# Performance work log

Hardware: AMD Instinct MI355X
Metric: run time of the kernel (lower is better)

Reference implementation:

```python
import jax, jax.numpy as jnp
import numpy as np

H, W = 4096, 4096
KH, KW = 3, 3


def setup_inputs() -> dict:
    key = jax.random.key(0)
    k1, k2, k3 = jax.random.split(key, 3)
    X = jax.random.normal(k1, (H, W), dtype=jnp.float32)
    weight = jax.random.normal(k2, (KH, KW), dtype=jnp.float32)
    bias = jax.random.normal(k3, (1,), dtype=jnp.float32)
    return {"X": X, "weight": weight, "bias": bias}


def reference(X, weight, bias):
    # Valid 2D cross-correlation (no kernel flip), matching the torch double loop:
    # Y[i, j] = sum(X[i:i+h, j:j+w] * K) + bias
    lhs = X[None, None, :, :]          # NCHW
    rhs = weight[None, None, :, :]     # OIHW
    out = jax.lax.conv_general_dilated(
        lhs, rhs,
        window_strides=(1, 1),
        padding="VALID",
        dimension_numbers=("NCHW", "OIHW", "NCHW"),
    )
    return out[0, 0] + bias[0]  # [H-KH+1, W-KW+1]
```

## Files before the change

### kernel.cpp

```cpp
#include <hip/hip_runtime.h>


constexpr int Hin = 4096;
constexpr int Win = 4096;
constexpr int OH  = 4094;
constexpr int OW  = 4094;

constexpr int C = 8;
constexpr int R = 4;
constexpr int CT = 512;
constexpr int RT = 1024;

__global__ __launch_bounds__(256, 4) void conv3x3_kernel(
    const float* __restrict__ X, const float* __restrict__ Wt,
    const float* __restrict__ B, float* __restrict__ Out)
{
    int nb = gridDim.x;
    int b  = blockIdx.x;
    int b2 = (b & 7) * (nb >> 3) + (b >> 3);

    int t   = b2 * 256 + threadIdx.x;
    int cid = t & (CT - 1);
    int rid = t >> 9;
    int c0  = cid * C;
    int r0  = rid * R;

    int q2off = (c0 + 8 <= Win - 4) ? (c0 + 8) : (Win - 4);

    float4 q[6][3];
#pragma unroll
    for (int ir = 0; ir < 6; ++ir) {
        int rr = r0 + ir;
        if (rr > Hin - 1) rr = Hin - 1;
        const float* row = X + (size_t)rr * Win;
        q[ir][0] = *reinterpret_cast<const float4*>(row + c0);
        q[ir][1] = *reinterpret_cast<const float4*>(row + c0 + 4);
        q[ir][2] = *reinterpret_cast<const float4*>(row + q2off);
    }

    float w[9];
#pragma unroll
    for (int i = 0; i < 9; ++i) w[i] = Wt[i];
    const float bias = B[0];

    float acc[R][C];
#pragma unroll
    for (int i = 0; i < R; ++i)
#pragma unroll
        for (int j = 0; j < C; ++j) acc[i][j] = bias;

#pragma unroll
    for (int ir = 0; ir < 6; ++ir) {
        float v[12] = {q[ir][0].x, q[ir][0].y, q[ir][0].z, q[ir][0].w,
                       q[ir][1].x, q[ir][1].y, q[ir][1].z, q[ir][1].w,
                       q[ir][2].x, q[ir][2].y, q[ir][2].z, q[ir][2].w};
#pragma unroll
        for (int kh = 0; kh < 3; ++kh) {
            int orr = ir - kh;
            if (orr >= 0 && orr < R) {
#pragma unroll
                for (int kw = 0; kw < 3; ++kw) {
                    float wv = w[kh * 3 + kw];
#pragma unroll
                    for (int j = 0; j < C; ++j)
                        acc[orr][j] = fmaf(v[j + kw], wv, acc[orr][j]);
                }
            }
        }
    }

#pragma unroll
    for (int i = 0; i < R; ++i) {
        int orow = r0 + i;
        if (orow < OH) {
            size_t o = (size_t)orow * OW + c0;
#pragma unroll
            for (int p = 0; p < C / 2; ++p) {
                int col = c0 + 2 * p;
                if (col < OW) {
                    *reinterpret_cast<float2*>(Out + o + 2 * p) =
                        make_float2(acc[i][2 * p], acc[i][2 * p + 1]);
                }
            }
        }
    }
}

extern "C" void kernel_launch(void* const* d_in, const int* in_sizes, int n_in,
                              void* d_out, int out_size, void* d_ws, size_t ws_size,
                              hipStream_t stream) {
    const float* X  = (const float*)d_in[0];
    const float* Wt = (const float*)d_in[1];
    const float* B  = (const float*)d_in[2];
    float* Out      = (float*)d_out;

    int total_threads = CT * RT;
    int blocks = total_threads / 256;
    conv3x3_kernel<<<blocks, 256, 0, stream>>>(X, Wt, B, Out);
}
```

Measured before the change: 30.05 us.

## Retile conv so each lane computes 2 columns by 8 rows with float2 loads

Changes the per-thread tile from 8 columns by 4 rows to 2 columns by 8 rows. A wave of 64 lanes now covers 128 contiguous columns using float2 loads, so each warp-level load instruction touches fully contiguous memory. Rows are split by block index, with 8 column-blocks by 512 row-blocks. The row halo overhead drops from 6/4 to 10/8 rows loaded per output row. The column halo grows from 12/8 to 4/2 elements loaded per output column, which adds redundant loads that should mostly hit cache, and the narrower accesses may make stores less efficient.

```diff
diff --git a/kernel.cpp b/kernel.cpp
--- a/kernel.cpp
+++ b/kernel.cpp
@@ -6,10 +6,7 @@
 constexpr int OH  = 4094;
 constexpr int OW  = 4094;
 
-constexpr int C = 8;
-constexpr int R = 4;
-constexpr int CT = 512;
-constexpr int RT = 1024;
+constexpr int R = 8;
 
 __global__ __launch_bounds__(256, 4) void conv3x3_kernel(
     const float* __restrict__ X, const float* __restrict__ Wt,
@@ -19,23 +16,24 @@
     int b  = blockIdx.x;
     int b2 = (b & 7) * (nb >> 3) + (b >> 3);
 
-    int t   = b2 * 256 + threadIdx.x;
-    int cid = t & (CT - 1);
-    int rid = t >> 9;
-    int c0  = cid * C;
-    int r0  = rid * R;
+    int bx   = b2 >> 9;
+    int by   = b2 & 511;
+    int wave = threadIdx.x >> 6;
+    int lane = threadIdx.x & 63;
 
-    int q2off = (c0 + 8 <= Win - 4) ? (c0 + 8) : (Win - 4);
+    int c  = bx * 512 + wave * 128 + 2 * lane;
+    int r0 = by * R;
 
-    float4 q[6][3];
+    int v1c = (c + 2 <= Win - 2) ? (c + 2) : (Win - 2);
+
+    float2 v0[R + 2], v1[R + 2];
 #pragma unroll
-    for (int ir = 0; ir < 6; ++ir) {
+    for (int ir = 0; ir < R + 2; ++ir) {
         int rr = r0 + ir;
         if (rr > Hin - 1) rr = Hin - 1;
         const float* row = X + (size_t)rr * Win;
-        q[ir][0] = *reinterpret_cast<const float4*>(row + c0);
-        q[ir][1] = *reinterpret_cast<const float4*>(row + c0 + 4);
-        q[ir][2] = *reinterpret_cast<const float4*>(row + q2off);
+        v0[ir] = *reinterpret_cast<const float2*>(row + c);
+        v1[ir] = *reinterpret_cast<const float2*>(row + v1c);
     }
 
     float w[9];
@@ -43,44 +41,31 @@
     for (int i = 0; i < 9; ++i) w[i] = Wt[i];
     const float bias = B[0];
 
-    float acc[R][C];
+    float2 acc[R];
 #pragma unroll
-    for (int i = 0; i < R; ++i)
-#pragma unroll
-        for (int j = 0; j < C; ++j) acc[i][j] = bias;
+    for (int i = 0; i < R; ++i) { acc[i].x = bias; acc[i].y = bias; }
 
 #pragma unroll
-    for (int ir = 0; ir < 6; ++ir) {
-        float v[12] = {q[ir][0].x, q[ir][0].y, q[ir][0].z, q[ir][0].w,
-                       q[ir][1].x, q[ir][1].y, q[ir][1].z, q[ir][1].w,
-                       q[ir][2].x, q[ir][2].y, q[ir][2].z, q[ir][2].w};
+    for (int i = 0; i < R; ++i) {
 #pragma unroll
         for (int kh = 0; kh < 3; ++kh) {
-            int orr = ir - kh;
-            if (orr >= 0 && orr < R) {
-#pragma unroll
-                for (int kw = 0; kw < 3; ++kw) {
-                    float wv = w[kh * 3 + kw];
-#pragma unroll
-                    for (int j = 0; j < C; ++j)
-                        acc[orr][j] = fmaf(v[j + kw], wv, acc[orr][j]);
-                }
-            }
+            int ir = i + kh;
+            float w0 = w[kh * 3 + 0], w1 = w[kh * 3 + 1], w2 = w[kh * 3 + 2];
+            acc[i].x = fmaf(v0[ir].x, w0, acc[i].x);
+            acc[i].x = fmaf(v0[ir].y, w1, acc[i].x);
+            acc[i].x = fmaf(v1[ir].x, w2, acc[i].x);
+            acc[i].y = fmaf(v0[ir].y, w0, acc[i].y);
+            acc[i].y = fmaf(v1[ir].x, w1, acc[i].y);
+            acc[i].y = fmaf(v1[ir].y, w2, acc[i].y);
         }
     }
 
+    if (c < OW) {
 #pragma unroll
-    for (int i = 0; i < R; ++i) {
-        int orow = r0 + i;
-        if (orow < OH) {
-            size_t o = (size_t)orow * OW + c0;
-#pragma unroll
-            for (int p = 0; p < C / 2; ++p) {
-                int col = c0 + 2 * p;
-                if (col < OW) {
-                    *reinterpret_cast<float2*>(Out + o + 2 * p) =
-                        make_float2(acc[i][2 * p], acc[i][2 * p + 1]);
-                }
+        for (int i = 0; i < R; ++i) {
+            int orow = r0 + i;
+            if (orow < OH) {
+                *reinterpret_cast<float2*>(Out + (size_t)orow * OW + c) = acc[i];
             }
         }
     }
@@ -94,7 +79,6 @@
     const float* B  = (const float*)d_in[2];
     float* Out      = (float*)d_out;
 
-    int total_threads = CT * RT;
-    int blocks = total_threads / 256;
+    int blocks = 8 * 512;
     conv3x3_kernel<<<blocks, 256, 0, stream>>>(X, Wt, B, Out);
 }
```

Result: faster. 26.32 us (-12.4%).
